# Optimization experiments

Measured on AMD Instinct MI355X. Metric: run time of the kernel, lower is better.

The kernel has to match this reference:

```python
import jax, jax.numpy as jnp
import numpy as np

T_TYPES, N_ARGS, N_MAPS = 15, 73, 3
D, H, FF = 512, 8, 512
N_TOK = 3071
LN_EPS = 1e-5


def setup_inputs() -> dict:
    key = jax.random.key(0)
    ks = jax.random.split(key, 32)
    s = 0.02
    p = lambda i, shape: (jax.random.normal(ks[i], shape, dtype=jnp.float32) * s)
    inp = {
        'subtask_index_history': jax.random.randint(ks[0], (N_TOK,), 0, T_TYPES * N_ARGS * N_MAPS, dtype=jnp.int32),
        'seq_masks': jax.random.randint(ks[1], (N_TOK,), 0, 64, dtype=jnp.int32),
        'Wt': p(2, (D, T_TYPES)), 'bt': p(3, (D,)),
        'Wa': p(4, (D, N_ARGS)), 'ba': p(5, (D,)),
        'Wm': p(6, (D, N_MAPS)), 'bm': p(7, (D,)),
        'sos': jnp.zeros((D,), dtype=jnp.float32),
        'Wq': p(8, (D, D)), 'bq': p(9, (D,)),
        'Wk': p(10, (D, D)), 'bk': p(11, (D,)),
        'Wv': p(12, (D, D)), 'bv': p(13, (D,)),
        'Wo': p(14, (D, D)), 'bo': p(15, (D,)),
        'W1': p(16, (FF, D)), 'b1': p(17, (FF,)),
        'W2': p(18, (D, FF)), 'b2': p(19, (D,)),
        'g1': jnp.ones((D,), jnp.float32), 'be1': jnp.zeros((D,), jnp.float32),
        'g2': jnp.ones((D,), jnp.float32), 'be2': jnp.zeros((D,), jnp.float32),
    }
    return inp


def _layer_norm(x, g, b):
    mu = jnp.mean(x, axis=-1, keepdims=True)
    var = jnp.mean((x - mu) ** 2, axis=-1, keepdims=True)
    return (x - mu) * jax.lax.rsqrt(var + LN_EPS) * g + b


def _enc_layer(x, mask, Wq, bq, Wk, bk, Wv, bv, Wo, bo, W1, b1, W2, b2, g1, be1, g2, be2):
    # x: [L, D]; mask: [L, L] additive (0 / -inf). inputs_are_labels=True -> no attn residual.
    L = x.shape[0]
    dh = D // H
    q = (x @ Wq.T + bq).reshape(L, H, dh)
    k = (x @ Wk.T + bk).reshape(L, H, dh)
    v = (x @ Wv.T + bv).reshape(L, H, dh)
    scores = jnp.einsum('ihd,jhd->hij', q, k) / np.sqrt(dh) + mask[None]  # [H, L, L]
    pr = jax.nn.softmax(scores, axis=-1)
    o = jnp.einsum('hij,jhd->ihd', pr, v).reshape(L, D)
    a = o @ Wo.T + bo
    xa = _layer_norm(a, g1, be1)
    y = jax.nn.leaky_relu(xa @ W1.T + b1) @ W2.T + b2
    return _layer_norm(xa + y, g2, be2)


def reference(subtask_index_history, seq_masks, Wt, bt, Wa, ba, Wm, bm, sos,
              Wq, bq, Wk, bk, Wv, bv, Wo, bo, W1, b1, W2, b2, g1, be1, g2, be2):
    idx = subtask_index_history
    t = idx // (N_ARGS * N_MAPS)
    a = (idx // N_MAPS) % N_ARGS
    m = idx % N_MAPS
    # one-hot @ Linear == embedding gather + bias
    emb = (Wt.T[t] + bt) + (Wa.T[a] + ba) + (Wm.T[m] + bm)  # [N, D]
    x = jnp.concatenate([sos[None, :], emb], axis=0)  # [L, D]
    L = x.shape[0]
    batch_ids = jnp.cumsum((seq_masks == 0).astype(jnp.int32))
    bid = jnp.concatenate([jnp.array([-1], jnp.int32), batch_ids])  # SOS gets unique id
    ar = jnp.arange(L)
    allowed = (ar[None, :] == 0) | ((bid[:, None] == bid[None, :]) & (ar[None, :] < ar[:, None]))
    mask = jnp.where(allowed, 0.0, -jnp.inf).astype(jnp.float32)
    lp = (Wq, bq, Wk, bk, Wv, bv, Wo, bo, W1, b1, W2, b2, g1, be1, g2, be2)
    # original reuses transformer_layer_a for both calls
    x = _enc_layer(x, mask, *lp)
    x = _enc_layer(x, mask, *lp)
    return x
```

## Files before the change

kernel.cpp:

```cpp
#include <hip/hip_runtime.h>

typedef unsigned short ushort_t;
typedef unsigned int uint_t;

#define L_TOK 3072
#define DMODEL 512
#define WELEM 262144

using bf16x8 = __attribute__((ext_vector_type(8))) short;
using f32x4  = __attribute__((ext_vector_type(4))) float;

__device__ __forceinline__ float b2f(ushort_t u) {
    union { uint_t i; float f; } c; c.i = ((uint_t)u) << 16; return c.f;
}
__device__ __forceinline__ ushort_t f2b(float f) {
    union { float f; uint_t i; } c; c.f = f;
    uint_t x = c.i;
    return (ushort_t)((x + 0x7fffu + ((x >> 16) & 1u)) >> 16);
}

__global__ __launch_bounds__(256) void prologue_kernel(
    const float* __restrict__ Wq, const float* __restrict__ Wk, const float* __restrict__ Wv,
    const float* __restrict__ Wo, const float* __restrict__ W1, const float* __restrict__ W2,
    ushort_t* __restrict__ WB,
    const int* __restrict__ idx,
    const float* __restrict__ Wt, const float* __restrict__ bt,
    const float* __restrict__ Wa, const float* __restrict__ ba,
    const float* __restrict__ Wm, const float* __restrict__ bm,
    const float* __restrict__ sos, ushort_t* __restrict__ X,
    const int* __restrict__ seq, int* __restrict__ start)
{
    __shared__ int sbuf0[256];
    __shared__ int sbuf1[256];
    int bid = blockIdx.x;
    int tid = threadIdx.x;

    if (bid < 1536) {
        int gid = bid * 256 + tid;
        int mat = gid >> 16;
        int off = (gid & 65535) * 4;
        const float* src;
        switch (mat) {
            case 0: src = Wq; break;
            case 1: src = Wk; break;
            case 2: src = Wv; break;
            case 3: src = Wo; break;
            case 4: src = W1; break;
            default: src = W2; break;
        }
        float4 v = *reinterpret_cast<const float4*>(src + off);
        uint2 o;
        o.x = (uint_t)f2b(v.x) | ((uint_t)f2b(v.y) << 16);
        o.y = (uint_t)f2b(v.z) | ((uint_t)f2b(v.w) << 16);
        *reinterpret_cast<uint2*>(&WB[mat * WELEM + off]) = o;
    } else if (bid < 7680) {
        int gid = (bid - 1536) * 256 + tid;
        int tok = gid >> 9;
        int d = gid & 511;
        float val;
        if (tok == 0) {
            val = sos[d];
        } else {
            int id = idx[tok - 1];
            int t = id / 219;
            int a = (id / 3) % 73;
            int m = id % 3;
            val = Wt[d * 15 + t] + bt[d]
                + Wa[d * 73 + a] + ba[d]
                + Wm[d * 3 + m] + bm[d];
        }
        X[gid] = f2b(val);
    } else {
        int carry = 0;
        for (int c = 0; c < 12; c++) {
            int i = c * 256 + tid;
            int b;
            if (i <= 1) b = i;
            else b = (seq[i - 1] == 0) ? i : 0;
            sbuf0[tid] = b;
            __syncthreads();
            int* src = sbuf0;
            int* dst = sbuf1;
            for (int off = 1; off < 256; off <<= 1) {
                int v = src[tid];
                if (tid >= off) { int u = src[tid - off]; if (u > v) v = u; }
                dst[tid] = v;
                __syncthreads();
                int* t = src; src = dst; dst = t;
            }
            int val = src[tid] > carry ? src[tid] : carry;
            start[i] = val;
            int tot = src[255] > carry ? src[255] : carry;
            __syncthreads();
            carry = tot;
        }
    }
}

template<int RELU>
__global__ __launch_bounds__(256) void gemm512(
    const ushort_t* __restrict__ A,
    const ushort_t* __restrict__ Wp0, const ushort_t* __restrict__ Wp1, const ushort_t* __restrict__ Wp2,
    const float* __restrict__ bp0, const float* __restrict__ bp1, const float* __restrict__ bp2,
    ushort_t* __restrict__ Cp0, ushort_t* __restrict__ Cp1, ushort_t* __restrict__ Cp2)
{
    const ushort_t* W = Wp0; const float* bias = bp0; ushort_t* C = Cp0;
    if (blockIdx.z == 1) { W = Wp1; bias = bp1; C = Cp1; }
    else if (blockIdx.z == 2) { W = Wp2; bias = bp2; C = Cp2; }

    __shared__ ushort_t As[2 * 32 * 72];
    __shared__ ushort_t Bs[2 * 64 * 72];

    const int tid = threadIdx.x;
    const int lane = tid & 63;
    const int w = tid >> 6;
    const int lm = lane & 15;
    const int q4 = lane >> 4;
    const int r0 = (w & 1) * 16;
    const int c0 = (w >> 1) * 32;

    const int m0 = blockIdx.x * 32;
    const int n0 = blockIdx.y * 64;

    const int srow = tid >> 3;
    const int scol = (tid & 7) << 3;
    const ushort_t* Arow = A + (size_t)(m0 + srow) * 512 + scol;
    const ushort_t* Brow0 = W + (size_t)(n0 + srow) * 512 + scol;
    const ushort_t* Brow1 = Brow0 + (size_t)32 * 512;
    const int ldsA = srow * 72 + scol;
    const int ldsB0 = srow * 72 + scol;
    const int ldsB1 = (srow + 32) * 72 + scol;

    f32x4 acc[2];
    acc[0] = (f32x4){0.f, 0.f, 0.f, 0.f};
    acc[1] = (f32x4){0.f, 0.f, 0.f, 0.f};

    uint4 a0 = *reinterpret_cast<const uint4*>(Arow);
    uint4 b0 = *reinterpret_cast<const uint4*>(Brow0);
    uint4 b1 = *reinterpret_cast<const uint4*>(Brow1);
    *reinterpret_cast<uint4*>(&As[ldsA]) = a0;
    *reinterpret_cast<uint4*>(&Bs[ldsB0]) = b0;
    *reinterpret_cast<uint4*>(&Bs[ldsB1]) = b1;
    __syncthreads();

#pragma unroll
    for (int it = 0; it < 8; it++) {
        const int curA = (it & 1) * 2304;
        const int altA = ((it & 1) ^ 1) * 2304;
        const int curB = (it & 1) * 4608;
        const int altB = ((it & 1) ^ 1) * 4608;
        const int nxt = (it + 1) * 64;

        uint4 na, nb0, nb1;
        if (it < 7) {
            na = *reinterpret_cast<const uint4*>(Arow + nxt);
            nb0 = *reinterpret_cast<const uint4*>(Brow0 + nxt);
            nb1 = *reinterpret_cast<const uint4*>(Brow1 + nxt);
        }

#pragma unroll
        for (int kk = 0; kk < 64; kk += 32) {
            bf16x8 af = *reinterpret_cast<const bf16x8*>(&As[curA + (r0 + lm) * 72 + kk + q4 * 8]);
#pragma unroll
            for (int nt = 0; nt < 2; nt++) {
                bf16x8 bf = *reinterpret_cast<const bf16x8*>(&Bs[curB + (c0 + nt * 16 + lm) * 72 + kk + q4 * 8]);
                acc[nt] = __builtin_amdgcn_mfma_f32_16x16x32_bf16(af, bf, acc[nt], 0, 0, 0);
            }
        }

        if (it < 7) {
            *reinterpret_cast<uint4*>(&As[altA + ldsA]) = na;
            *reinterpret_cast<uint4*>(&Bs[altB + ldsB0]) = nb0;
            *reinterpret_cast<uint4*>(&Bs[altB + ldsB1]) = nb1;
            __syncthreads();
        }
    }

#pragma unroll
    for (int nt = 0; nt < 2; nt++) {
        int col = n0 + c0 + nt * 16 + lm;
        float bv = bias[col];
#pragma unroll
        for (int r = 0; r < 4; r++) {
            int row = m0 + r0 + q4 * 4 + r;
            float v = acc[nt][r] + bv;
            if (RELU) v = (v > 0.f) ? v : 0.01f * v;
            C[(size_t)row * 512 + col] = f2b(v);
        }
    }
}

__global__ __launch_bounds__(256) void attn_mfma(
    const ushort_t* __restrict__ Q, const ushort_t* __restrict__ K,
    const ushort_t* __restrict__ V, const int* __restrict__ START,
    ushort_t* __restrict__ O)
{
    __shared__ ushort_t VtS[4][64 * 72];
    __shared__ ushort_t PsS[4][16 * 72];

    int w = threadIdx.x >> 6;
    int lane = threadIdx.x & 63;
    ushort_t* Vt = VtS[w];
    ushort_t* Ps = PsS[w];

    int gw = blockIdx.x * 4 + w;
    int tile = 191 - (gw >> 3);
    int h = gw & 7;
    int i0 = tile * 16;
    int lm = lane & 15;
    int q4 = lane >> 4;

    int iq0 = i0 + q4 * 4;
    int sq[4];
#pragma unroll
    for (int r = 0; r < 4; r++) sq[r] = START[iq0 + r];

    int lo = START[i0]; if (lo < 1) lo = 1;
    int nk = i0 + 16 - lo;

    const ushort_t* Qp = Q + (size_t)(i0 + lm) * 512 + h * 64 + q4 * 8;
    bf16x8 aQ0 = *reinterpret_cast<const bf16x8*>(Qp);
    bf16x8 aQ1 = *reinterpret_cast<const bf16x8*>(Qp + 32);

    float m_run[4], l_run[4];
    f32x4 oacc[4];
#pragma unroll
    for (int r = 0; r < 4; r++) { m_run[r] = -INFINITY; l_run[r] = 0.f; }
#pragma unroll
    for (int nt = 0; nt < 4; nt++) oacc[nt] = (f32x4){0.f, 0.f, 0.f, 0.f};

    for (int t0 = 0; t0 < nk; t0 += 64) {
        int tv = t0 + lane;
        int jv = (tv == 0) ? 0 : (lo + tv - 1);
        if (jv > L_TOK - 1) jv = L_TOK - 1;
        const uint4* vp = reinterpret_cast<const uint4*>(&V[(size_t)jv * 512 + h * 64]);
        uint4 vr[8];
#pragma unroll
        for (int c = 0; c < 8; c++) vr[c] = vp[c];

        int jn[4];
#pragma unroll
        for (int nt = 0; nt < 4; nt++) {
            int t = t0 + nt * 16 + lm;
            jn[nt] = (t == 0) ? 0 : (lo + t - 1);
        }
        f32x4 sacc[4];
#pragma unroll
        for (int nt = 0; nt < 4; nt++) sacc[nt] = (f32x4){0.f, 0.f, 0.f, 0.f};
#pragma unroll
        for (int nt = 0; nt < 4; nt++) {
            int jc = jn[nt] > L_TOK - 1 ? L_TOK - 1 : jn[nt];
            const ushort_t* Kp = K + (size_t)jc * 512 + h * 64 + q4 * 8;
            bf16x8 bK0 = *reinterpret_cast<const bf16x8*>(Kp);
            bf16x8 bK1 = *reinterpret_cast<const bf16x8*>(Kp + 32);
            sacc[nt] = __builtin_amdgcn_mfma_f32_16x16x32_bf16(aQ0, bK0, sacc[nt], 0, 0, 0);
            sacc[nt] = __builtin_amdgcn_mfma_f32_16x16x32_bf16(aQ1, bK1, sacc[nt], 0, 0, 0);
        }

#pragma unroll
        for (int c = 0; c < 8; c++) {
            uint_t ww[4] = {vr[c].x, vr[c].y, vr[c].z, vr[c].w};
#pragma unroll
            for (int e = 0; e < 4; e++) {
                int d0 = c * 8 + e * 2;
                Vt[d0 * 72 + lane] = (ushort_t)(ww[e] & 0xffffu);
                Vt[(d0 + 1) * 72 + lane] = (ushort_t)(ww[e] >> 16);
            }
        }

#pragma unroll
        for (int nt = 0; nt < 4; nt++) {
            int jju = jn[nt];
#pragma unroll
            for (int r = 0; r < 4; r++) {
                float s = sacc[nt][r] * 0.125f;
                bool val = (jju == 0) || (sq[r] <= jju && jju < iq0 + r);
                sacc[nt][r] = val ? s : -INFINITY;
            }
        }

        float mnew[4], alpha[4];
#pragma unroll
        for (int r = 0; r < 4; r++) {
            float mx = fmaxf(fmaxf(sacc[0][r], sacc[1][r]), fmaxf(sacc[2][r], sacc[3][r]));
            mx = fmaxf(mx, __shfl_xor(mx, 1));
            mx = fmaxf(mx, __shfl_xor(mx, 2));
            mx = fmaxf(mx, __shfl_xor(mx, 4));
            mx = fmaxf(mx, __shfl_xor(mx, 8));
            float mn = fmaxf(m_run[r], mx);
            mnew[r] = mn;
            alpha[r] = __expf(m_run[r] - mn);
        }

#pragma unroll
        for (int r = 0; r < 4; r++) {
            float rs = 0.f;
#pragma unroll
            for (int nt = 0; nt < 4; nt++) {
                float p = __expf(sacc[nt][r] - mnew[r]);
                rs += p;
                Ps[(q4 * 4 + r) * 72 + nt * 16 + lm] = f2b(p);
            }
            rs += __shfl_xor(rs, 1);
            rs += __shfl_xor(rs, 2);
            rs += __shfl_xor(rs, 4);
            rs += __shfl_xor(rs, 8);
            l_run[r] = l_run[r] * alpha[r] + rs;
            m_run[r] = mnew[r];
        }
#pragma unroll
        for (int nt = 0; nt < 4; nt++)
#pragma unroll
            for (int r = 0; r < 4; r++) oacc[nt][r] *= alpha[r];

        bf16x8 aP0 = *reinterpret_cast<const bf16x8*>(&Ps[lm * 72 + q4 * 8]);
        bf16x8 aP1 = *reinterpret_cast<const bf16x8*>(&Ps[lm * 72 + 32 + q4 * 8]);
#pragma unroll
        for (int nt = 0; nt < 4; nt++) {
            bf16x8 bV0 = *reinterpret_cast<const bf16x8*>(&Vt[(nt * 16 + lm) * 72 + q4 * 8]);
            bf16x8 bV1 = *reinterpret_cast<const bf16x8*>(&Vt[(nt * 16 + lm) * 72 + 32 + q4 * 8]);
            oacc[nt] = __builtin_amdgcn_mfma_f32_16x16x32_bf16(aP0, bV0, oacc[nt], 0, 0, 0);
            oacc[nt] = __builtin_amdgcn_mfma_f32_16x16x32_bf16(aP1, bV1, oacc[nt], 0, 0, 0);
        }
    }

#pragma unroll
    for (int r = 0; r < 4; r++) {
        float inv = (l_run[r] > 0.f) ? (1.f / l_run[r]) : 0.f;
#pragma unroll
        for (int nt = 0; nt < 4; nt++)
            O[(size_t)(iq0 + r) * 512 + h * 64 + nt * 16 + lm] = f2b(oacc[nt][r] * inv);
    }
}

template<int RESID, int F32OUT>
__global__ __launch_bounds__(256) void ln_kernel(
    const ushort_t* __restrict__ X, const ushort_t* __restrict__ R,
    const float* __restrict__ g, const float* __restrict__ be,
    void* __restrict__ outv)
{
    int tok = blockIdx.x * 4 + (threadIdx.x >> 6);
    int lane = threadIdx.x & 63;
    size_t base = (size_t)tok * 512 + lane * 8;

    float v[8];
    {
        uint4 ux = *reinterpret_cast<const uint4*>(&X[base]);
        uint_t ua[4] = {ux.x, ux.y, ux.z, ux.w};
#pragma unroll
        for (int p = 0; p < 4; p++) {
            v[2 * p] = b2f((ushort_t)(ua[p] & 0xffffu));
            v[2 * p + 1] = b2f((ushort_t)(ua[p] >> 16));
        }
        if (RESID) {
            uint4 ur = *reinterpret_cast<const uint4*>(&R[base]);
            uint_t ub[4] = {ur.x, ur.y, ur.z, ur.w};
#pragma unroll
            for (int p = 0; p < 4; p++) {
                v[2 * p] += b2f((ushort_t)(ub[p] & 0xffffu));
                v[2 * p + 1] += b2f((ushort_t)(ub[p] >> 16));
            }
        }
    }
    float sum = 0.f;
#pragma unroll
    for (int j = 0; j < 8; j++) sum += v[j];
#pragma unroll
    for (int off = 32; off > 0; off >>= 1) sum += __shfl_xor(sum, off);
    float mu = sum * (1.f / 512.f);
    float var = 0.f;
#pragma unroll
    for (int j = 0; j < 8; j++) { float d = v[j] - mu; var += d * d; }
#pragma unroll
    for (int off = 32; off > 0; off >>= 1) var += __shfl_xor(var, off);
    float rstd = rsqrtf(var * (1.f / 512.f) + 1e-5f);

    const float4* gp = reinterpret_cast<const float4*>(g);
    const float4* bp = reinterpret_cast<const float4*>(be);
    float4 g0 = gp[2 * lane], g1 = gp[2 * lane + 1];
    float4 b0 = bp[2 * lane], b1 = bp[2 * lane + 1];
    float gg[8] = {g0.x, g0.y, g0.z, g0.w, g1.x, g1.y, g1.z, g1.w};
    float bb[8] = {b0.x, b0.y, b0.z, b0.w, b1.x, b1.y, b1.z, b1.w};

    float o[8];
#pragma unroll
    for (int j = 0; j < 8; j++) o[j] = (v[j] - mu) * rstd * gg[j] + bb[j];

    if (F32OUT) {
        float* outf = (float*)outv;
        float4 o0 = {o[0], o[1], o[2], o[3]};
        float4 o1 = {o[4], o[5], o[6], o[7]};
        *reinterpret_cast<float4*>(&outf[base]) = o0;
        *reinterpret_cast<float4*>(&outf[base + 4]) = o1;
    } else {
        ushort_t* outb = (ushort_t*)outv;
        uint_t outp[4];
#pragma unroll
        for (int p = 0; p < 4; p++)
            outp[p] = (uint_t)f2b(o[2 * p]) | ((uint_t)f2b(o[2 * p + 1]) << 16);
        uint4 ov; ov.x = outp[0]; ov.y = outp[1]; ov.z = outp[2]; ov.w = outp[3];
        *reinterpret_cast<uint4*>(&outb[base]) = ov;
    }
}

extern "C" void kernel_launch(void* const* d_in, const int* in_sizes, int n_in,
                              void* d_out, int out_size, void* d_ws, size_t ws_size,
                              hipStream_t stream) {
    const int*   idx = (const int*)d_in[0];
    const int*   seq = (const int*)d_in[1];
    const float* Wt  = (const float*)d_in[2];
    const float* bt  = (const float*)d_in[3];
    const float* Wa  = (const float*)d_in[4];
    const float* ba  = (const float*)d_in[5];
    const float* Wm  = (const float*)d_in[6];
    const float* bm  = (const float*)d_in[7];
    const float* sos = (const float*)d_in[8];
    const float* Wq  = (const float*)d_in[9];
    const float* bq  = (const float*)d_in[10];
    const float* Wk  = (const float*)d_in[11];
    const float* bk  = (const float*)d_in[12];
    const float* Wv  = (const float*)d_in[13];
    const float* bv  = (const float*)d_in[14];
    const float* Wo  = (const float*)d_in[15];
    const float* bo  = (const float*)d_in[16];
    const float* W1  = (const float*)d_in[17];
    const float* b1  = (const float*)d_in[18];
    const float* W2  = (const float*)d_in[19];
    const float* b2  = (const float*)d_in[20];
    const float* g1  = (const float*)d_in[21];
    const float* be1 = (const float*)d_in[22];
    const float* g2  = (const float*)d_in[23];
    const float* be2 = (const float*)d_in[24];

    const size_t NB = (size_t)L_TOK * DMODEL;

    int* START = (int*)d_ws;
    ushort_t* WB = (ushort_t*)d_ws + 16384;
    ushort_t* WQc = WB + 0 * WELEM;
    ushort_t* WKc = WB + 1 * WELEM;
    ushort_t* WVc = WB + 2 * WELEM;
    ushort_t* WOc = WB + 3 * WELEM;
    ushort_t* W1c = WB + 4 * WELEM;
    ushort_t* W2c = WB + 5 * WELEM;
    ushort_t* bufs = WB + 6 * WELEM;
    ushort_t* B0 = bufs;
    ushort_t* B1 = bufs + 1 * NB;
    ushort_t* B2 = bufs + 2 * NB;
    ushort_t* B3 = bufs + 3 * NB;

    prologue_kernel<<<7681, 256, 0, stream>>>(
        Wq, Wk, Wv, Wo, W1, W2, WB,
        idx, Wt, bt, Wa, ba, Wm, bm, sos, B0,
        seq, START);

    for (int layer = 0; layer < 2; layer++) {
        gemm512<0><<<dim3(96, 8, 3), 256, 0, stream>>>(B0, WQc, WKc, WVc, bq, bk, bv, B1, B2, B3);
        attn_mfma<<<384, 256, 0, stream>>>(B1, B2, B3, START, B0);
        gemm512<0><<<dim3(96, 8, 1), 256, 0, stream>>>(B0, WOc, WOc, WOc, bo, bo, bo, B1, B1, B1);
        ln_kernel<0, 0><<<768, 256, 0, stream>>>(B1, B1, g1, be1, B2);
        gemm512<1><<<dim3(96, 8, 1), 256, 0, stream>>>(B2, W1c, W1c, W1c, b1, b1, b1, B1, B1, B1);
        gemm512<0><<<dim3(96, 8, 1), 256, 0, stream>>>(B1, W2c, W2c, W2c, b2, b2, b2, B3, B3, B3);
        if (layer == 0)
            ln_kernel<1, 0><<<768, 256, 0, stream>>>(B3, B2, g2, be2, B0);
        else
            ln_kernel<1, 1><<<768, 256, 0, stream>>>(B3, B2, g2, be2, d_out);
    }
}
```

Measured before the change: 253.6 us.

## Fuse LayerNorm1 into FFN1 GEMM prologue and recompute it in final LN

Removes the standalone LN1 kernel. The first FFN GEMM now loads its 32-row A tile into LDS, normalizes it in place, then runs the MFMA loop with leaky-ReLU. The final LN kernel recomputes LN1 from the attention-output projection before adding the FFN output and applying LN2, so the normalized activation never goes to global memory. Attention also moves to 128-thread blocks (2 waves each, twice as many blocks) for finer scheduling. The cost is redundant LN1 work in every N-tile block plus a recompute in the final kernel, and a larger LDS footprint per GEMM block.

Measured after the change: 266.5 us. +5.1%, slower.

```diff
diff --git a/kernel.cpp b/kernel.cpp
--- a/kernel.cpp
+++ b/kernel.cpp
@@ -190,20 +190,162 @@
     }
 }
 
-__global__ __launch_bounds__(256) void attn_mfma(
+__global__ __launch_bounds__(256) void gemm_ln_relu(
+    const ushort_t* __restrict__ A, const ushort_t* __restrict__ W,
+    const float* __restrict__ g, const float* __restrict__ be,
+    const float* __restrict__ bias, ushort_t* __restrict__ C)
+{
+    __shared__ ushort_t As[32 * 520];
+    __shared__ ushort_t Bs[2 * 64 * 72];
+
+    const int tid = threadIdx.x;
+    const int lane = tid & 63;
+    const int w = tid >> 6;
+    const int lm = lane & 15;
+    const int q4 = lane >> 4;
+    const int r0 = (w & 1) * 16;
+    const int c0 = (w >> 1) * 32;
+
+    const int m0 = blockIdx.x * 32;
+    const int n0 = blockIdx.y * 64;
+
+    const int arow = tid >> 3;
+    const int jcol = tid & 7;
+    {
+        const ushort_t* Ap = A + (size_t)(m0 + arow) * 512 + jcol * 8;
+#pragma unroll
+        for (int c = 0; c < 8; c++) {
+            uint4 v = *reinterpret_cast<const uint4*>(Ap + c * 64);
+            *reinterpret_cast<uint4*>(&As[arow * 520 + jcol * 8 + c * 64]) = v;
+        }
+    }
+    const int srow = tid >> 3;
+    const int scol = (tid & 7) << 3;
+    const ushort_t* Brow0 = W + (size_t)(n0 + srow) * 512 + scol;
+    const ushort_t* Brow1 = Brow0 + (size_t)32 * 512;
+    const int ldsB0 = srow * 72 + scol;
+    const int ldsB1 = (srow + 32) * 72 + scol;
+    {
+        uint4 b0 = *reinterpret_cast<const uint4*>(Brow0);
+        uint4 b1 = *reinterpret_cast<const uint4*>(Brow1);
+        *reinterpret_cast<uint4*>(&Bs[ldsB0]) = b0;
+        *reinterpret_cast<uint4*>(&Bs[ldsB1]) = b1;
+    }
+    __syncthreads();
+
+    {
+        ushort_t* rp = &As[arow * 520 + jcol * 64];
+        uint4 raw[8];
+#pragma unroll
+        for (int c = 0; c < 8; c++) raw[c] = *reinterpret_cast<const uint4*>(rp + c * 8);
+        float sum = 0.f;
+#pragma unroll
+        for (int c = 0; c < 8; c++) {
+            uint_t uu[4] = {raw[c].x, raw[c].y, raw[c].z, raw[c].w};
+#pragma unroll
+            for (int e = 0; e < 4; e++)
+                sum += b2f((ushort_t)(uu[e] & 0xffffu)) + b2f((ushort_t)(uu[e] >> 16));
+        }
+#pragma unroll
+        for (int off = 1; off < 8; off <<= 1) sum += __shfl_xor(sum, off);
+        float mu = sum * (1.f / 512.f);
+        float var = 0.f;
+#pragma unroll
+        for (int c = 0; c < 8; c++) {
+            uint_t uu[4] = {raw[c].x, raw[c].y, raw[c].z, raw[c].w};
+#pragma unroll
+            for (int e = 0; e < 4; e++) {
+                float d0 = b2f((ushort_t)(uu[e] & 0xffffu)) - mu;
+                float d1 = b2f((ushort_t)(uu[e] >> 16)) - mu;
+                var += d0 * d0 + d1 * d1;
+            }
+        }
+#pragma unroll
+        for (int off = 1; off < 8; off <<= 1) var += __shfl_xor(var, off);
+        float rstd = rsqrtf(var * (1.f / 512.f) + 1e-5f);
+
+        const float* gp = g + jcol * 64;
+        const float* bp = be + jcol * 64;
+#pragma unroll
+        for (int c = 0; c < 8; c++) {
+            uint_t uu[4] = {raw[c].x, raw[c].y, raw[c].z, raw[c].w};
+            uint_t outw[4];
+#pragma unroll
+            for (int e = 0; e < 4; e++) {
+                int d0 = c * 8 + e * 2;
+                float x0 = b2f((ushort_t)(uu[e] & 0xffffu));
+                float x1 = b2f((ushort_t)(uu[e] >> 16));
+                float y0 = (x0 - mu) * rstd * gp[d0] + bp[d0];
+                float y1 = (x1 - mu) * rstd * gp[d0 + 1] + bp[d0 + 1];
+                outw[e] = (uint_t)f2b(y0) | ((uint_t)f2b(y1) << 16);
+            }
+            uint4 ov; ov.x = outw[0]; ov.y = outw[1]; ov.z = outw[2]; ov.w = outw[3];
+            *reinterpret_cast<uint4*>(rp + c * 8) = ov;
+        }
+    }
+    __syncthreads();
+
+    f32x4 acc[2];
+    acc[0] = (f32x4){0.f, 0.f, 0.f, 0.f};
+    acc[1] = (f32x4){0.f, 0.f, 0.f, 0.f};
+
+#pragma unroll
+    for (int it = 0; it < 8; it++) {
+        const int curB = (it & 1) * 4608;
+        const int altB = ((it & 1) ^ 1) * 4608;
+        const int nxt = (it + 1) * 64;
+
+        uint4 nb0, nb1;
+        if (it < 7) {
+            nb0 = *reinterpret_cast<const uint4*>(Brow0 + nxt);
+            nb1 = *reinterpret_cast<const uint4*>(Brow1 + nxt);
+        }
+
+#pragma unroll
+        for (int kk = 0; kk < 64; kk += 32) {
+            bf16x8 af = *reinterpret_cast<const bf16x8*>(&As[(r0 + lm) * 520 + it * 64 + kk + q4 * 8]);
+#pragma unroll
+            for (int nt = 0; nt < 2; nt++) {
+                bf16x8 bf = *reinterpret_cast<const bf16x8*>(&Bs[curB + (c0 + nt * 16 + lm) * 72 + kk + q4 * 8]);
+                acc[nt] = __builtin_amdgcn_mfma_f32_16x16x32_bf16(af, bf, acc[nt], 0, 0, 0);
+            }
+        }
+
+        if (it < 7) {
+            *reinterpret_cast<uint4*>(&Bs[altB + ldsB0]) = nb0;
+            *reinterpret_cast<uint4*>(&Bs[altB + ldsB1]) = nb1;
+            __syncthreads();
+        }
+    }
+
+#pragma unroll
+    for (int nt = 0; nt < 2; nt++) {
+        int col = n0 + c0 + nt * 16 + lm;
+        float bv = bias[col];
+#pragma unroll
+        for (int r = 0; r < 4; r++) {
+            int row = m0 + r0 + q4 * 4 + r;
+            float v = acc[nt][r] + bv;
+            v = (v > 0.f) ? v : 0.01f * v;
+            C[(size_t)row * 512 + col] = f2b(v);
+        }
+    }
+}
+
+__global__ __launch_bounds__(128) void attn_mfma(
     const ushort_t* __restrict__ Q, const ushort_t* __restrict__ K,
     const ushort_t* __restrict__ V, const int* __restrict__ START,
     ushort_t* __restrict__ O)
 {
-    __shared__ ushort_t VtS[4][64 * 72];
-    __shared__ ushort_t PsS[4][16 * 72];
+    __shared__ ushort_t VtS[2][64 * 72];
+    __shared__ ushort_t PsS[2][16 * 72];
 
     int w = threadIdx.x >> 6;
     int lane = threadIdx.x & 63;
     ushort_t* Vt = VtS[w];
     ushort_t* Ps = PsS[w];
 
-    int gw = blockIdx.x * 4 + w;
+    int gw = blockIdx.x * 2 + w;
     int tile = 191 - (gw >> 3);
     int h = gw & 7;
     int i0 = tile * 16;
@@ -333,58 +475,82 @@
     }
 }
 
-template<int RESID, int F32OUT>
-__global__ __launch_bounds__(256) void ln_kernel(
-    const ushort_t* __restrict__ X, const ushort_t* __restrict__ R,
-    const float* __restrict__ g, const float* __restrict__ be,
+template<int F32OUT>
+__global__ __launch_bounds__(256) void ln2_fused(
+    const ushort_t* __restrict__ Aop, const ushort_t* __restrict__ Y,
+    const float* __restrict__ g1, const float* __restrict__ be1,
+    const float* __restrict__ g2, const float* __restrict__ be2,
     void* __restrict__ outv)
 {
     int tok = blockIdx.x * 4 + (threadIdx.x >> 6);
     int lane = threadIdx.x & 63;
     size_t base = (size_t)tok * 512 + lane * 8;
 
-    float v[8];
+    float a[8];
     {
-        uint4 ux = *reinterpret_cast<const uint4*>(&X[base]);
+        uint4 ux = *reinterpret_cast<const uint4*>(&Aop[base]);
         uint_t ua[4] = {ux.x, ux.y, ux.z, ux.w};
 #pragma unroll
         for (int p = 0; p < 4; p++) {
-            v[2 * p] = b2f((ushort_t)(ua[p] & 0xffffu));
-            v[2 * p + 1] = b2f((ushort_t)(ua[p] >> 16));
-        }
-        if (RESID) {
-            uint4 ur = *reinterpret_cast<const uint4*>(&R[base]);
-            uint_t ub[4] = {ur.x, ur.y, ur.z, ur.w};
-#pragma unroll
-            for (int p = 0; p < 4; p++) {
-                v[2 * p] += b2f((ushort_t)(ub[p] & 0xffffu));
-                v[2 * p + 1] += b2f((ushort_t)(ub[p] >> 16));
-            }
+            a[2 * p] = b2f((ushort_t)(ua[p] & 0xffffu));
+            a[2 * p + 1] = b2f((ushort_t)(ua[p] >> 16));
         }
     }
     float sum = 0.f;
 #pragma unroll
-    for (int j = 0; j < 8; j++) sum += v[j];
+    for (int j = 0; j < 8; j++) sum += a[j];
 #pragma unroll
     for (int off = 32; off > 0; off >>= 1) sum += __shfl_xor(sum, off);
     float mu = sum * (1.f / 512.f);
     float var = 0.f;
 #pragma unroll
-    for (int j = 0; j < 8; j++) { float d = v[j] - mu; var += d * d; }
+    for (int j = 0; j < 8; j++) { float d = a[j] - mu; var += d * d; }
 #pragma unroll
     for (int off = 32; off > 0; off >>= 1) var += __shfl_xor(var, off);
     float rstd = rsqrtf(var * (1.f / 512.f) + 1e-5f);
 
-    const float4* gp = reinterpret_cast<const float4*>(g);
-    const float4* bp = reinterpret_cast<const float4*>(be);
-    float4 g0 = gp[2 * lane], g1 = gp[2 * lane + 1];
-    float4 b0 = bp[2 * lane], b1 = bp[2 * lane + 1];
-    float gg[8] = {g0.x, g0.y, g0.z, g0.w, g1.x, g1.y, g1.z, g1.w};
-    float bb[8] = {b0.x, b0.y, b0.z, b0.w, b1.x, b1.y, b1.z, b1.w};
+    const float4* g1p = reinterpret_cast<const float4*>(g1);
+    const float4* b1p = reinterpret_cast<const float4*>(be1);
+    float4 g1a = g1p[2 * lane], g1b = g1p[2 * lane + 1];
+    float4 b1a = b1p[2 * lane], b1b = b1p[2 * lane + 1];
+    float gg1[8] = {g1a.x, g1a.y, g1a.z, g1a.w, g1b.x, g1b.y, g1b.z, g1b.w};
+    float bb1[8] = {b1a.x, b1a.y, b1a.z, b1a.w, b1b.x, b1b.y, b1b.z, b1b.w};
+
+    float v[8];
+    {
+        uint4 uy = *reinterpret_cast<const uint4*>(&Y[base]);
+        uint_t ub[4] = {uy.x, uy.y, uy.z, uy.w};
+#pragma unroll
+        for (int p = 0; p < 4; p++) {
+            float xa0 = b2f(f2b((a[2 * p] - mu) * rstd * gg1[2 * p] + bb1[2 * p]));
+            float xa1 = b2f(f2b((a[2 * p + 1] - mu) * rstd * gg1[2 * p + 1] + bb1[2 * p + 1]));
+            v[2 * p] = xa0 + b2f((ushort_t)(ub[p] & 0xffffu));
+            v[2 * p + 1] = xa1 + b2f((ushort_t)(ub[p] >> 16));
+        }
+    }
+    float sum2 = 0.f;
+#pragma unroll
+    for (int j = 0; j < 8; j++) sum2 += v[j];
+#pragma unroll
+    for (int off = 32; off > 0; off >>= 1) sum2 += __shfl_xor(sum2, off);
+    float mu2 = sum2 * (1.f / 512.f);
+    float var2 = 0.f;
+#pragma unroll
+    for (int j = 0; j < 8; j++) { float d = v[j] - mu2; var2 += d * d; }
+#pragma unroll
+    for (int off = 32; off > 0; off >>= 1) var2 += __shfl_xor(var2, off);
+    float rstd2 = rsqrtf(var2 * (1.f / 512.f) + 1e-5f);
+
+    const float4* g2p = reinterpret_cast<const float4*>(g2);
+    const float4* b2p = reinterpret_cast<const float4*>(be2);
+    float4 g2a = g2p[2 * lane], g2b = g2p[2 * lane + 1];
+    float4 b2a = b2p[2 * lane], b2b = b2p[2 * lane + 1];
+    float gg2[8] = {g2a.x, g2a.y, g2a.z, g2a.w, g2b.x, g2b.y, g2b.z, g2b.w};
+    float bb2[8] = {b2a.x, b2a.y, b2a.z, b2a.w, b2b.x, b2b.y, b2b.z, b2b.w};
 
     float o[8];
 #pragma unroll
-    for (int j = 0; j < 8; j++) o[j] = (v[j] - mu) * rstd * gg[j] + bb[j];
+    for (int j = 0; j < 8; j++) o[j] = (v[j] - mu2) * rstd2 * gg2[j] + bb2[j];
 
     if (F32OUT) {
         float* outf = (float*)outv;
@@ -455,14 +621,13 @@
 
     for (int layer = 0; layer < 2; layer++) {
         gemm512<0><<<dim3(96, 8, 3), 256, 0, stream>>>(B0, WQc, WKc, WVc, bq, bk, bv, B1, B2, B3);
-        attn_mfma<<<384, 256, 0, stream>>>(B1, B2, B3, START, B0);
+        attn_mfma<<<768, 128, 0, stream>>>(B1, B2, B3, START, B0);
         gemm512<0><<<dim3(96, 8, 1), 256, 0, stream>>>(B0, WOc, WOc, WOc, bo, bo, bo, B1, B1, B1);
-        ln_kernel<0, 0><<<768, 256, 0, stream>>>(B1, B1, g1, be1, B2);
-        gemm512<1><<<dim3(96, 8, 1), 256, 0, stream>>>(B2, W1c, W1c, W1c, b1, b1, b1, B1, B1, B1);
-        gemm512<0><<<dim3(96, 8, 1), 256, 0, stream>>>(B1, W2c, W2c, W2c, b2, b2, b2, B3, B3, B3);
+        gemm_ln_relu<<<dim3(96, 8), 256, 0, stream>>>(B1, W1c, g1, be1, b1, B2);
+        gemm512<0><<<dim3(96, 8, 1), 256, 0, stream>>>(B2, W2c, W2c, W2c, b2, b2, b2, B3, B3, B3);
         if (layer == 0)
-            ln_kernel<1, 0><<<768, 256, 0, stream>>>(B3, B2, g2, be2, B0);
+            ln2_fused<0><<<768, 256, 0, stream>>>(B1, B3, g1, be1, g2, be2, B0);
         else
-            ln_kernel<1, 1><<<768, 256, 0, stream>>>(B3, B2, g2, be2, d_out);
-    }
-}
+            ln2_fused<1><<<768, 256, 0, stream>>>(B1, B3, g1, be1, g2, be2, d_out);
+    }
+}
```

## Store V transposed from QKV GEMM and read it directly in attention

Applied to the files above, without the earlier changes.

The QKV projection GEMM now writes the V output transposed as [D][L]. This lets the attention kernel load MFMA B-operands for P·V straight from global memory instead of staging and transposing V through per-wave LDS each tile. The SOS key (token 0) is also peeled out: its score and value seed the online-softmax state, so the key loop starts at the segment start and no longer needs special-case index mapping. In exchange, the V GEMM epilogue does strided transposed stores. The attention kernel also issues vector loads at arbitrary token offsets, which may be unaligned and can read up to a tile past the end of each row.

After: 274.0 us. 1.08x slower.

```diff
diff --git a/kernel.cpp b/kernel.cpp
--- a/kernel.cpp
+++ b/kernel.cpp
@@ -97,7 +97,7 @@
     }
 }
 
-template<int RELU>
+template<int RELU, int TRANSV>
 __global__ __launch_bounds__(256) void gemm512(
     const ushort_t* __restrict__ A,
     const ushort_t* __restrict__ Wp0, const ushort_t* __restrict__ Wp1, const ushort_t* __restrict__ Wp2,
@@ -176,6 +176,7 @@
         }
     }
 
+    const bool transv = TRANSV && (blockIdx.z == 2);
 #pragma unroll
     for (int nt = 0; nt < 2; nt++) {
         int col = n0 + c0 + nt * 16 + lm;
@@ -185,22 +186,23 @@
             int row = m0 + r0 + q4 * 4 + r;
             float v = acc[nt][r] + bv;
             if (RELU) v = (v > 0.f) ? v : 0.01f * v;
-            C[(size_t)row * 512 + col] = f2b(v);
+            if (transv)
+                C[(size_t)col * L_TOK + row] = f2b(v);
+            else
+                C[(size_t)row * 512 + col] = f2b(v);
         }
     }
 }
 
 __global__ __launch_bounds__(256) void attn_mfma(
     const ushort_t* __restrict__ Q, const ushort_t* __restrict__ K,
-    const ushort_t* __restrict__ V, const int* __restrict__ START,
+    const ushort_t* __restrict__ VT, const int* __restrict__ START,
     ushort_t* __restrict__ O)
 {
-    __shared__ ushort_t VtS[4][64 * 72];
     __shared__ ushort_t PsS[4][16 * 72];
 
     int w = threadIdx.x >> 6;
     int lane = threadIdx.x & 63;
-    ushort_t* Vt = VtS[w];
     ushort_t* Ps = PsS[w];
 
     int gw = blockIdx.x * 4 + w;
@@ -216,40 +218,49 @@
     for (int r = 0; r < 4; r++) sq[r] = START[iq0 + r];
 
     int lo = START[i0]; if (lo < 1) lo = 1;
-    int nk = i0 + 16 - lo;
+    const int kend = i0 + 15;
 
     const ushort_t* Qp = Q + (size_t)(i0 + lm) * 512 + h * 64 + q4 * 8;
     bf16x8 aQ0 = *reinterpret_cast<const bf16x8*>(Qp);
     bf16x8 aQ1 = *reinterpret_cast<const bf16x8*>(Qp + 32);
 
+    float s0 = 0.f;
+    {
+        bf16x8 k00 = *reinterpret_cast<const bf16x8*>(K + h * 64 + q4 * 8);
+        bf16x8 k01 = *reinterpret_cast<const bf16x8*>(K + h * 64 + 32 + q4 * 8);
+#pragma unroll
+        for (int j = 0; j < 8; j++) {
+            s0 += b2f((ushort_t)aQ0[j]) * b2f((ushort_t)k00[j]);
+            s0 += b2f((ushort_t)aQ1[j]) * b2f((ushort_t)k01[j]);
+        }
+        s0 += __shfl_xor(s0, 16);
+        s0 += __shfl_xor(s0, 32);
+        s0 *= 0.125f;
+    }
+
+    const ushort_t* VTh = VT + (size_t)h * 64 * L_TOK;
     float m_run[4], l_run[4];
     f32x4 oacc[4];
 #pragma unroll
-    for (int r = 0; r < 4; r++) { m_run[r] = -INFINITY; l_run[r] = 0.f; }
-#pragma unroll
-    for (int nt = 0; nt < 4; nt++) oacc[nt] = (f32x4){0.f, 0.f, 0.f, 0.f};
-
-    for (int t0 = 0; t0 < nk; t0 += 64) {
-        int tv = t0 + lane;
-        int jv = (tv == 0) ? 0 : (lo + tv - 1);
-        if (jv > L_TOK - 1) jv = L_TOK - 1;
-        const uint4* vp = reinterpret_cast<const uint4*>(&V[(size_t)jv * 512 + h * 64]);
-        uint4 vr[8];
-#pragma unroll
-        for (int c = 0; c < 8; c++) vr[c] = vp[c];
-
-        int jn[4];
+    for (int nt = 0; nt < 4; nt++) {
+        float v0 = b2f(VTh[(size_t)(nt * 16 + lm) * L_TOK]);
+#pragma unroll
+        for (int r = 0; r < 4; r++) oacc[nt][r] = v0;
+    }
+#pragma unroll
+    for (int r = 0; r < 4; r++) {
+        m_run[r] = __shfl(s0, q4 * 4 + r);
+        l_run[r] = 1.f;
+    }
+
+    for (int t0 = lo; t0 < kend; t0 += 64) {
+        f32x4 sacc[4];
+#pragma unroll
+        for (int nt = 0; nt < 4; nt++) sacc[nt] = (f32x4){0.f, 0.f, 0.f, 0.f};
 #pragma unroll
         for (int nt = 0; nt < 4; nt++) {
-            int t = t0 + nt * 16 + lm;
-            jn[nt] = (t == 0) ? 0 : (lo + t - 1);
-        }
-        f32x4 sacc[4];
-#pragma unroll
-        for (int nt = 0; nt < 4; nt++) sacc[nt] = (f32x4){0.f, 0.f, 0.f, 0.f};
-#pragma unroll
-        for (int nt = 0; nt < 4; nt++) {
-            int jc = jn[nt] > L_TOK - 1 ? L_TOK - 1 : jn[nt];
+            int j = t0 + nt * 16 + lm;
+            int jc = j > L_TOK - 1 ? L_TOK - 1 : j;
             const ushort_t* Kp = K + (size_t)jc * 512 + h * 64 + q4 * 8;
             bf16x8 bK0 = *reinterpret_cast<const bf16x8*>(Kp);
             bf16x8 bK1 = *reinterpret_cast<const bf16x8*>(Kp + 32);
@@ -258,23 +269,12 @@
         }
 
 #pragma unroll
-        for (int c = 0; c < 8; c++) {
-            uint_t ww[4] = {vr[c].x, vr[c].y, vr[c].z, vr[c].w};
-#pragma unroll
-            for (int e = 0; e < 4; e++) {
-                int d0 = c * 8 + e * 2;
-                Vt[d0 * 72 + lane] = (ushort_t)(ww[e] & 0xffffu);
-                Vt[(d0 + 1) * 72 + lane] = (ushort_t)(ww[e] >> 16);
-            }
-        }
-
-#pragma unroll
         for (int nt = 0; nt < 4; nt++) {
-            int jju = jn[nt];
+            int j = t0 + nt * 16 + lm;
 #pragma unroll
             for (int r = 0; r < 4; r++) {
                 float s = sacc[nt][r] * 0.125f;
-                bool val = (jju == 0) || (sq[r] <= jju && jju < iq0 + r);
+                bool val = (sq[r] <= j) && (j < iq0 + r);
                 sacc[nt][r] = val ? s : -INFINITY;
             }
         }
@@ -317,8 +317,9 @@
         bf16x8 aP1 = *reinterpret_cast<const bf16x8*>(&Ps[lm * 72 + 32 + q4 * 8]);
 #pragma unroll
         for (int nt = 0; nt < 4; nt++) {
-            bf16x8 bV0 = *reinterpret_cast<const bf16x8*>(&Vt[(nt * 16 + lm) * 72 + q4 * 8]);
-            bf16x8 bV1 = *reinterpret_cast<const bf16x8*>(&Vt[(nt * 16 + lm) * 72 + 32 + q4 * 8]);
+            const ushort_t* vp = VTh + (size_t)(nt * 16 + lm) * L_TOK + t0;
+            bf16x8 bV0 = *reinterpret_cast<const bf16x8*>(vp + q4 * 8);
+            bf16x8 bV1 = *reinterpret_cast<const bf16x8*>(vp + 32 + q4 * 8);
             oacc[nt] = __builtin_amdgcn_mfma_f32_16x16x32_bf16(aP0, bV0, oacc[nt], 0, 0, 0);
             oacc[nt] = __builtin_amdgcn_mfma_f32_16x16x32_bf16(aP1, bV1, oacc[nt], 0, 0, 0);
         }
@@ -454,12 +455,12 @@
         seq, START);
 
     for (int layer = 0; layer < 2; layer++) {
-        gemm512<0><<<dim3(96, 8, 3), 256, 0, stream>>>(B0, WQc, WKc, WVc, bq, bk, bv, B1, B2, B3);
+        gemm512<0, 1><<<dim3(96, 8, 3), 256, 0, stream>>>(B0, WQc, WKc, WVc, bq, bk, bv, B1, B2, B3);
         attn_mfma<<<384, 256, 0, stream>>>(B1, B2, B3, START, B0);
-        gemm512<0><<<dim3(96, 8, 1), 256, 0, stream>>>(B0, WOc, WOc, WOc, bo, bo, bo, B1, B1, B1);
+        gemm512<0, 0><<<dim3(96, 8, 1), 256, 0, stream>>>(B0, WOc, WOc, WOc, bo, bo, bo, B1, B1, B1);
         ln_kernel<0, 0><<<768, 256, 0, stream>>>(B1, B1, g1, be1, B2);
-        gemm512<1><<<dim3(96, 8, 1), 256, 0, stream>>>(B2, W1c, W1c, W1c, b1, b1, b1, B1, B1, B1);
-        gemm512<0><<<dim3(96, 8, 1), 256, 0, stream>>>(B1, W2c, W2c, W2c, b2, b2, b2, B3, B3, B3);
+        gemm512<1, 0><<<dim3(96, 8, 1), 256, 0, stream>>>(B2, W1c, W1c, W1c, b1, b1, b1, B1, B1, B1);
+        gemm512<0, 0><<<dim3(96, 8, 1), 256, 0, stream>>>(B1, W2c, W2c, W2c, b2, b2, b2, B3, B3, B3);
         if (layer == 0)
             ln_kernel<1, 0><<<768, 256, 0, stream>>>(B3, B2, g2, be2, B0);
         else
```
